# Optimization experiments

Measured on AMD Instinct MI355X. Metric: run time of the kernel, lower is better.

## Reference

```python
import jax, jax.numpy as jnp
import numpy as np

K = 5            # neighbors
TEMP = 1.0       # softmax temperature
BANK = 1000      # fixed bank capacity in source
B = 65536        # batch
D = 256          # feature_dim
EPS = 1e-12      # F.normalize eps


def _l2norm(x):
    # F.normalize(x, dim=1): x / max(||x||, eps)
    n = jnp.sqrt(jnp.sum(x * x, axis=1, keepdims=True))
    return x / jnp.maximum(n, EPS)


def setup_inputs() -> dict:
    key = jax.random.key(0)
    k1, k2, k3, k4 = jax.random.split(key, 4)
    features = jax.random.normal(k1, (B, D), dtype=jnp.float32)
    feature_bank = jax.random.normal(k2, (BANK, D), dtype=jnp.float32)
    # fusion_layer: Linear(2D -> D), ReLU, Linear(D -> D). torch weight layout [out, in].
    W1 = jax.random.normal(k3, (D, 2 * D), dtype=jnp.float32) * (1.0 / np.sqrt(2 * D))
    b1 = jnp.zeros((D,), dtype=jnp.float32)
    W2 = jax.random.normal(k4, (D, D), dtype=jnp.float32) * (1.0 / np.sqrt(D))
    b2 = jnp.zeros((D,), dtype=jnp.float32)
    return {"features": features, "feature_bank": feature_bank,
            "W1": W1, "b1": b1, "W2": W2, "b2": b2}


def reference(features, feature_bank, W1, b1, W2, b2):
    # knn_search: cosine similarity against the (full) bank
    qn = _l2norm(features)                      # [B, D]
    bn = _l2norm(feature_bank)                  # [BANK, D]
    sims = qn @ bn.T                            # [B, BANK]
    top_s, top_i = jax.lax.top_k(sims, K)       # [B, K]
    w = jax.nn.softmax(top_s / TEMP, axis=1)    # [B, K]
    neigh = feature_bank[top_i]                 # gather -> [B, K, D]
    nf = jnp.einsum('bkd,bk->bd', neigh, w)     # weighted average of neighbors
    # fusion MLP on concat([query, neighbors])
    fused = jnp.concatenate([features, nf], axis=1)    # [B, 2D]
    h = jax.nn.relu(fused @ W1.T + b1)                 # [B, D]
    out = h @ W2.T + b2                                # [B, D]
    return out
```

## Files before the change

### kernel.cpp

```cpp
#include <hip/hip_runtime.h>

#define DIM 256
#define NC 12

typedef __attribute__((ext_vector_type(8))) short short8;
typedef __attribute__((ext_vector_type(4))) float f32x4;

__device__ __forceinline__ short f32bf(float f) {
    unsigned u = __builtin_bit_cast(unsigned, f);
    unsigned r = u + 0x7FFFu + ((u >> 16) & 1u);
    return (short)(r >> 16);
}

__device__ __forceinline__ void gld_lds16(const void* g, void* l) {
    __builtin_amdgcn_global_load_lds((const __attribute__((address_space(1))) unsigned int*)g,
                                     (__attribute__((address_space(3))) unsigned int*)l, 16, 0, 0);
}

template<int CTRL>
__device__ __forceinline__ unsigned dppmax(unsigned x) {
    unsigned y = (unsigned)__builtin_amdgcn_update_dpp(0, (int)x, CTRL, 0xF, 0xF, true);
    return x > y ? x : y;
}

__global__ __launch_bounds__(256) void k_prep(const float* __restrict__ bank,
        const float* __restrict__ W1, const float* __restrict__ W2,
        short* __restrict__ bnbf, double* __restrict__ binv,
        short* __restrict__ w1bf, short* __restrict__ w2bf)
{
    __shared__ double part[4];
    __shared__ double s_inv;
    const int bid = blockIdx.x, t = threadIdx.x;
    if (bid < 1024) {
        const int row = bid;
        if (row < 1000) {
            float v = bank[(size_t)row * DIM + t];
            double ssq = (double)v * (double)v;
            for (int o = 32; o > 0; o >>= 1) ssq += __shfl_down(ssq, o);
            if ((t & 63) == 0) part[t >> 6] = ssq;
            __syncthreads();
            if (t == 0) {
                double s = part[0] + part[1] + part[2] + part[3];
                double n = sqrt(s); if (n < 1e-12) n = 1e-12;
                double inv = 1.0 / n;
                binv[row] = inv; s_inv = inv;
            }
            __syncthreads();
            const int pcol = (((t >> 3) ^ (row & 7)) << 3) | (t & 7);
            bnbf[(size_t)row * DIM + pcol] = f32bf((float)((double)v * s_inv));
        } else {
            bnbf[(size_t)row * DIM + t] = 0;
            if (t == 0) binv[row] = 0.0;
        }
    } else if (bid < 1536) {
        const int i = (bid - 1024) * 256 + t;
        w1bf[i] = f32bf(W1[i]);
    } else {
        const int i = (bid - 1536) * 256 + t;
        w2bf[i] = f32bf(W2[i]);
    }
}

__global__ __launch_bounds__(256) void k_sims(const float* __restrict__ feat,
        const short* __restrict__ bnbf, short* __restrict__ sims, int qoff)
{
    __shared__ alignas(16) short Qs[64 * 264];
    __shared__ alignas(16) short Ab[64 * 256];
    const int t = threadIdx.x, lane = t & 63, w = t >> 6;
    const int n16 = lane & 15, q4 = lane >> 4;

    {
        const int r = t >> 2, p = t & 3;
        const float4* src = (const float4*)(feat + (size_t)(qoff + blockIdx.x * 64 + r) * DIM + p * 64);
        short* dst = Qs + r * 264 + p * 64;
        #pragma unroll
        for (int i = 0; i < 16; ++i) {
            float4 v = src[i];
            dst[i*4+0] = f32bf(v.x); dst[i*4+1] = f32bf(v.y);
            dst[i*4+2] = f32bf(v.z); dst[i*4+3] = f32bf(v.w);
        }
    }
    const char* gA = (const char*)bnbf;
    char* lA = (char*)Ab;
    #pragma unroll
    for (int i = 0; i < 8; ++i)
        gld_lds16(gA + i * 4096 + t * 16, lA + i * 4096 + (t >> 6) * 1024);
    __syncthreads();

    short8 bq[8][4];
    #pragma unroll
    for (int kc = 0; kc < 8; ++kc)
        #pragma unroll
        for (int nt = 0; nt < 4; ++nt)
            bq[kc][nt] = *(const short8*)(Qs + (nt * 16 + n16) * 264 + kc * 32 + q4 * 8);

    const int ml = w * 16 + n16;
    int aoff[8];
    #pragma unroll
    for (int kc = 0; kc < 8; ++kc)
        aoff[kc] = (ml * 256 + (((kc * 4 + q4) ^ (ml & 7)) << 3)) * 2;

    const f32x4 vzero = {0.f, 0.f, 0.f, 0.f};
    for (int chunk = 0; chunk < 16; ++chunk) {
        f32x4 acc[4];
        acc[0] = vzero; acc[1] = vzero; acc[2] = vzero; acc[3] = vzero;
        #pragma unroll
        for (int kc = 0; kc < 8; ++kc) {
            short8 af = *(const short8*)(lA + aoff[kc]);
            #pragma unroll
            for (int nt = 0; nt < 4; ++nt)
                acc[nt] = __builtin_amdgcn_mfma_f32_16x16x32_bf16(af, bq[kc][nt], acc[nt], 0, 0, 0);
        }
        const int bankb = chunk * 64 + w * 16 + q4 * 4;
        #pragma unroll
        for (int nt = 0; nt < 4; ++nt) {
            const int qc = blockIdx.x * 64 + nt * 16 + n16;
            uint2 u;
            u.x = ((unsigned)(unsigned short)f32bf(acc[nt][0])) |
                  (((unsigned)(unsigned short)f32bf(acc[nt][1])) << 16);
            u.y = ((unsigned)(unsigned short)f32bf(acc[nt][2])) |
                  (((unsigned)(unsigned short)f32bf(acc[nt][3])) << 16);
            *(uint2*)(sims + (size_t)qc * 1024 + bankb) = u;
        }
        __syncthreads();
        if (chunk < 15) {
            #pragma unroll
            for (int i = 0; i < 8; ++i)
                gld_lds16(gA + (size_t)(chunk + 1) * 32768 + i * 4096 + t * 16,
                          lA + i * 4096 + (t >> 6) * 1024);
            __syncthreads();
        }
    }
}

__global__ __launch_bounds__(256) void k_select(const short* __restrict__ sims,
        int* __restrict__ top, int qoff)
{
    const int t = threadIdx.x, lane = t & 63, w = t >> 6;
    const int q = blockIdx.x * 4 + w;
    const uint4* p = (const uint4*)(sims + (size_t)q * 1024 + lane * 16);
    uint4 a = p[0], b = p[1];

    unsigned k[16];
    {
        unsigned words[8] = {a.x, a.y, a.z, a.w, b.x, b.y, b.z, b.w};
        #pragma unroll
        for (int j = 0; j < 16; ++j) {
            unsigned h = (j & 1) ? (words[j >> 1] >> 16) : (words[j >> 1] & 0xFFFFu);
            unsigned m = (h ^ 0x8000u) ^ ((0u - (h >> 15)) & 0x7FFFu);
            int idx = lane * 16 + j;
            k[j] = (idx < 1000) ? ((m << 16) | (unsigned)idx) : 0u;
        }
    }
    #pragma unroll
    for (int sz = 2; sz <= 16; sz <<= 1)
        #pragma unroll
        for (int st = sz >> 1; st >= 1; st >>= 1)
            #pragma unroll
            for (int i = 0; i < 16; ++i) {
                int j = i ^ st;
                if (j > i) {
                    bool desc = ((i & sz) == 0);
                    unsigned lo = k[i], hi = k[j];
                    unsigned mx = lo > hi ? lo : hi;
                    unsigned mn = lo > hi ? hi : lo;
                    k[i] = desc ? mx : mn;
                    k[j] = desc ? mn : mx;
                }
            }
    unsigned mine = 0;
    #pragma unroll
    for (int r = 0; r < 12; ++r) {
        unsigned m = k[0];
        m = dppmax<0xB1>(m);
        m = dppmax<0x4E>(m);
        m = dppmax<0x141>(m);
        m = dppmax<0x140>(m);
        m = dppmax<0x142>(m);
        m = dppmax<0x143>(m);
        unsigned wm = (unsigned)__builtin_amdgcn_readlane((int)m, 63);
        if (lane == r) mine = wm;
        if (k[0] == wm) {
            #pragma unroll
            for (int s = 0; s < 12; ++s) k[s] = k[s + 1];
        }
    }
    if (lane < 12) top[(size_t)(qoff + q) * NC + lane] = (int)(mine & 0xFFFFu);
}

__global__ __launch_bounds__(256) void k_refine(const float* __restrict__ feat,
        const float* __restrict__ bank, const int* __restrict__ top,
        const double* __restrict__ binv, short* __restrict__ nf)
{
    const int t = threadIdx.x, lane = t & 63, w = t >> 6;
    const int g = lane >> 4, u = lane & 15;
    const int q = blockIdx.x * 16 + w * 4 + g;

    int ci[NC];
    #pragma unroll
    for (int c = 0; c < NC; ++c) ci[c] = top[(size_t)q * NC + c];
    double bd[NC];
    #pragma unroll
    for (int c = 0; c < NC; ++c) bd[c] = binv[ci[c]];

    float qf[16];
    float ssf = 0.f;
    #pragma unroll
    for (int j = 0; j < 4; ++j) {
        float4 v = *(const float4*)(feat + (size_t)q * DIM + j * 64 + u * 4);
        qf[j*4+0] = v.x; qf[j*4+1] = v.y; qf[j*4+2] = v.z; qf[j*4+3] = v.w;
        ssf += v.x*v.x + v.y*v.y + v.z*v.z + v.w*v.w;
    }
    #pragma unroll
    for (int o = 1; o < 16; o <<= 1) ssf += __shfl_xor(ssf, o, 16);
    float nq = sqrtf(ssf); if (nq < 1e-12f) nq = 1e-12f;
    const float qi = 1.f / nq;

    float s[NC];
    #pragma unroll
    for (int c = 0; c < NC; ++c) {
        const float* brow = bank + (size_t)ci[c] * DIM + u * 4;
        float a0 = 0.f, a1 = 0.f, a2 = 0.f, a3 = 0.f;
        #pragma unroll
        for (int j = 0; j < 4; ++j) {
            float4 b = *(const float4*)(brow + j * 64);
            a0 += qf[j*4+0] * b.x; a1 += qf[j*4+1] * b.y;
            a2 += qf[j*4+2] * b.z; a3 += qf[j*4+3] * b.w;
        }
        s[c] = (a0 + a1) + (a2 + a3);
    }
    #pragma unroll
    for (int o = 1; o < 16; o <<= 1)
        #pragma unroll
        for (int c = 0; c < NC; ++c) s[c] += __shfl_xor(s[c], o, 16);

    float vf[NC];
    unsigned long long key[NC];
    #pragma unroll
    for (int c = 0; c < NC; ++c) {
        float v = s[c] * qi * (float)bd[c];
        vf[c] = v;
        unsigned ub = __builtin_bit_cast(unsigned, v);
        unsigned m = (ub >> 31) ? ~ub : (ub | 0x80000000u);
        key[c] = ((unsigned long long)m << 10) | (unsigned long long)(1023 - ci[c]);
    }

    int rank[NC];
    #pragma unroll
    for (int c = 0; c < NC; ++c) rank[c] = 0;
    #pragma unroll
    for (int c1 = 0; c1 < NC; ++c1)
        #pragma unroll
        for (int c2 = c1 + 1; c2 < NC; ++c2) {
            const bool gt = key[c1] > key[c2];
            rank[c2] += gt ? 1 : 0;
            rank[c1] += gt ? 0 : 1;
        }

    float v5 = 0.f, v6 = 0.f;
    #pragma unroll
    for (int c = 0; c < NC; ++c) {
        v5 += (rank[c] == 4) ? vf[c] : 0.f;
        v6 += (rank[c] == 5) ? vf[c] : 0.f;
    }
    const int need = (v5 - v6) < 1e-5f;
    if (__any(need)) {
        double ssd = 0.0;
        #pragma unroll
        for (int j = 0; j < 16; ++j) ssd += (double)qf[j] * (double)qf[j];
        #pragma unroll
        for (int o = 1; o < 16; o <<= 1) ssd += __shfl_xor(ssd, o, 16);
        double nd = sqrt(ssd); if (nd < 1e-12) nd = 1e-12;
        const double qid = 1.0 / nd;
        double sd[NC];
        #pragma unroll
        for (int c = 0; c < NC; ++c) {
            const float* brow = bank + (size_t)ci[c] * DIM + u * 4;
            double a0 = 0, a1 = 0, a2 = 0, a3 = 0;
            #pragma unroll
            for (int j = 0; j < 4; ++j) {
                float4 b = *(const float4*)(brow + j * 64);
                a0 += (double)qf[j*4+0] * b.x; a1 += (double)qf[j*4+1] * b.y;
                a2 += (double)qf[j*4+2] * b.z; a3 += (double)qf[j*4+3] * b.w;
            }
            sd[c] = (a0 + a1) + (a2 + a3);
        }
        #pragma unroll
        for (int o = 1; o < 16; o <<= 1)
            #pragma unroll
            for (int c = 0; c < NC; ++c) sd[c] += __shfl_xor(sd[c], o, 16);
        #pragma unroll
        for (int c = 0; c < NC; ++c) {
            double vd = sd[c] * qid * bd[c];
            vf[c] = (float)vd;
            unsigned long long ub = __builtin_bit_cast(unsigned long long, vd);
            unsigned long long m = (ub >> 63) ? ~ub : (ub | 0x8000000000000000ULL);
            key[c] = (m & ~0x3FFULL) | (unsigned long long)(1023 - ci[c]);
        }
        #pragma unroll
        for (int c = 0; c < NC; ++c) rank[c] = 0;
        #pragma unroll
        for (int c1 = 0; c1 < NC; ++c1)
            #pragma unroll
            for (int c2 = c1 + 1; c2 < NC; ++c2) {
                const bool gt = key[c1] > key[c2];
                rank[c2] += gt ? 1 : 0;
                rank[c1] += gt ? 0 : 1;
            }
    }

    float vm = vf[0];
    #pragma unroll
    for (int c = 1; c < NC; ++c) vm = fmaxf(vm, vf[c]);
    float e[NC]; float wsum = 0.f;
    #pragma unroll
    for (int c = 0; c < NC; ++c) {
        float ex = __expf(vf[c] - vm);
        ex = (rank[c] < 5) ? ex : 0.f;
        e[c] = ex; wsum += ex;
    }
    const float inv = 1.f / wsum;

    int   selidx[5];
    float selw[5];
    #pragma unroll
    for (int k = 0; k < 5; ++k) {
        int idx = 0; float wv = 0.f;
        #pragma unroll
        for (int c = 0; c < NC; ++c) {
            const bool is = (rank[c] == k);
            idx += is ? ci[c] : 0;
            wv  += is ? e[c]  : 0.f;
        }
        selidx[k] = idx; selw[k] = wv * inv;
    }

    float4 oa[4];
    #pragma unroll
    for (int j = 0; j < 4; ++j) { oa[j].x = 0.f; oa[j].y = 0.f; oa[j].z = 0.f; oa[j].w = 0.f; }
    #pragma unroll
    for (int k = 0; k < 5; ++k) {
        const float wc = selw[k];
        const float* brow = bank + (size_t)selidx[k] * DIM + u * 4;
        #pragma unroll
        for (int j = 0; j < 4; ++j) {
            float4 b = *(const float4*)(brow + j * 64);
            oa[j].x += wc * b.x; oa[j].y += wc * b.y;
            oa[j].z += wc * b.z; oa[j].w += wc * b.w;
        }
    }
    short* od = nf + (size_t)q * DIM + u * 4;
    #pragma unroll
    for (int j = 0; j < 4; ++j) {
        uint2 pk;
        pk.x = ((unsigned)(unsigned short)f32bf(oa[j].x)) |
               (((unsigned)(unsigned short)f32bf(oa[j].y)) << 16);
        pk.y = ((unsigned)(unsigned short)f32bf(oa[j].z)) |
               (((unsigned)(unsigned short)f32bf(oa[j].w)) << 16);
        *(uint2*)(od + j * 64) = pk;
    }
}

__global__ __launch_bounds__(256) void k_mlp1(const float* __restrict__ feat,
        const short* __restrict__ nf, const short* __restrict__ w1bf,
        const float* __restrict__ b1, short* __restrict__ h)
{
    __shared__ alignas(16) short As[64 * 40];
    __shared__ alignas(16) short Bs[256 * 40];
    const int t = threadIdx.x, lane = t & 63, w = t >> 6;
    const int mb = blockIdx.x * 64;
    const int r = t >> 2, p = t & 3;
    const int n16 = lane & 15, ko = (lane >> 4) << 3;
    const f32x4 vzero = {0.f, 0.f, 0.f, 0.f};

    f32x4 acc[4][4];
    #pragma unroll
    for (int a = 0; a < 4; ++a)
        #pragma unroll
        for (int b = 0; b < 4; ++b) acc[a][b] = vzero;

    for (int kc = 0; kc < 16; ++kc) {
        short* ad = As + r * 40 + p * 8;
        if (kc < 8) {
            const float4* s = (const float4*)(feat + (size_t)(mb + r) * 256 + kc * 32 + p * 8);
            float4 v0 = s[0], v1 = s[1];
            ad[0] = f32bf(v0.x); ad[1] = f32bf(v0.y); ad[2] = f32bf(v0.z); ad[3] = f32bf(v0.w);
            ad[4] = f32bf(v1.x); ad[5] = f32bf(v1.y); ad[6] = f32bf(v1.z); ad[7] = f32bf(v1.w);
        } else {
            *(uint4*)ad = *(const uint4*)(nf + (size_t)(mb + r) * 256 + (kc - 8) * 32 + p * 8);
        }
        {
            const uint4* bsrc = (const uint4*)(w1bf + (size_t)t * 512 + kc * 32);
            short* bdst = Bs + t * 40;
            *(uint4*)(bdst +  0) = bsrc[0];
            *(uint4*)(bdst +  8) = bsrc[1];
            *(uint4*)(bdst + 16) = bsrc[2];
            *(uint4*)(bdst + 24) = bsrc[3];
        }
        __syncthreads();
        short8 af[4], bf[4];
        #pragma unroll
        for (int mt = 0; mt < 4; ++mt)
            af[mt] = *(const short8*)(As + (mt * 16 + n16) * 40 + ko);
        #pragma unroll
        for (int nt = 0; nt < 4; ++nt)
            bf[nt] = *(const short8*)(Bs + (w * 64 + nt * 16 + n16) * 40 + ko);
        #pragma unroll
        for (int mt = 0; mt < 4; ++mt)
            #pragma unroll
            for (int nt = 0; nt < 4; ++nt)
                acc[mt][nt] = __builtin_amdgcn_mfma_f32_16x16x32_bf16(af[mt], bf[nt], acc[mt][nt], 0, 0, 0);
        __syncthreads();
    }
    {
        const int rq = (lane >> 4) << 2;
        const int cc = lane & 15;
        #pragma unroll
        for (int mt = 0; mt < 4; ++mt)
            #pragma unroll
            for (int nt = 0; nt < 4; ++nt) {
                const int row = mb + mt * 16 + rq;
                const int col = w * 64 + nt * 16 + cc;
                const float bias = b1[col];
                #pragma unroll
                for (int rr = 0; rr < 4; ++rr) {
                    float v = acc[mt][nt][rr] + bias;
                    v = fmaxf(v, 0.f);
                    h[(size_t)(row + rr) * 256 + col] = f32bf(v);
                }
            }
    }
}

__global__ __launch_bounds__(256) void k_mlp2(const short* __restrict__ h,
        const short* __restrict__ w2bf, const float* __restrict__ b2,
        float* __restrict__ out)
{
    __shared__ alignas(16) short As[64 * 40];
    __shared__ alignas(16) short Bs[256 * 40];
    const int t = threadIdx.x, lane = t & 63, w = t >> 6;
    const int mb = blockIdx.x * 64;
    const int r = t >> 2, p = t & 3;
    const int n16 = lane & 15, ko = (lane >> 4) << 3;
    const f32x4 vzero = {0.f, 0.f, 0.f, 0.f};

    f32x4 acc[4][4];
    #pragma unroll
    for (int a = 0; a < 4; ++a)
        #pragma unroll
        for (int b = 0; b < 4; ++b) acc[a][b] = vzero;

    for (int kc = 0; kc < 8; ++kc) {
        *(uint4*)(As + r * 40 + p * 8) =
            *(const uint4*)(h + (size_t)(mb + r) * 256 + kc * 32 + p * 8);
        {
            const uint4* bsrc = (const uint4*)(w2bf + (size_t)t * 256 + kc * 32);
            short* bdst = Bs + t * 40;
            *(uint4*)(bdst +  0) = bsrc[0];
            *(uint4*)(bdst +  8) = bsrc[1];
            *(uint4*)(bdst + 16) = bsrc[2];
            *(uint4*)(bdst + 24) = bsrc[3];
        }
        __syncthreads();
        short8 af[4], bf[4];
        #pragma unroll
        for (int mt = 0; mt < 4; ++mt)
            af[mt] = *(const short8*)(As + (mt * 16 + n16) * 40 + ko);
        #pragma unroll
        for (int nt = 0; nt < 4; ++nt)
            bf[nt] = *(const short8*)(Bs + (w * 64 + nt * 16 + n16) * 40 + ko);
        #pragma unroll
        for (int mt = 0; mt < 4; ++mt)
            #pragma unroll
            for (int nt = 0; nt < 4; ++nt)
                acc[mt][nt] = __builtin_amdgcn_mfma_f32_16x16x32_bf16(af[mt], bf[nt], acc[mt][nt], 0, 0, 0);
        __syncthreads();
    }
    {
        const int rq = (lane >> 4) << 2;
        const int cc = lane & 15;
        #pragma unroll
        for (int mt = 0; mt < 4; ++mt)
            #pragma unroll
            for (int nt = 0; nt < 4; ++nt) {
                const int row = mb + mt * 16 + rq;
                const int col = w * 64 + nt * 16 + cc;
                const float bias = b2[col];
                #pragma unroll
                for (int rr = 0; rr < 4; ++rr)
                    out[(size_t)(row + rr) * 256 + col] = acc[mt][nt][rr] + bias;
            }
    }
}

extern "C" void kernel_launch(void* const* d_in, const int* in_sizes, int n_in,
                              void* d_out, int out_size, void* d_ws, size_t ws_size,
                              hipStream_t stream) {
    const float* feat = (const float*)d_in[0];
    const float* bank = (const float*)d_in[1];
    const float* W1   = (const float*)d_in[2];
    const float* b1   = (const float*)d_in[3];
    const float* W2   = (const float*)d_in[4];
    const float* b2   = (const float*)d_in[5];
    float* out = (float*)d_out;

    char* ws = (char*)d_ws;
    short*  bnbf = (short*)(ws + 0);
    double* binv = (double*)(ws + 524288);
    short*  w1bf = (short*)(ws + 532480);
    short*  w2bf = (short*)(ws + 794624);
    int*    top  = (int*)(ws + 925696);
    short*  nf   = (short*)(ws + 4071424);
    short*  X    = (short*)(ws + 37625856);

    k_prep<<<1792, 256, 0, stream>>>(bank, W1, W2, bnbf, binv, w1bf, w2bf);
    for (int s = 0; s < 4; ++s) {
        const int qoff = s * 16384;
        k_sims  <<<256,  256, 0, stream>>>(feat, bnbf, X, qoff);
        k_select<<<4096, 256, 0, stream>>>(X, top, qoff);
    }
    k_refine<<<4096, 256, 0, stream>>>(feat, bank, top, binv, nf);
    k_mlp1  <<<1024, 256, 0, stream>>>(feat, nf, w1bf, b1, (short*)X);
    k_mlp2  <<<1024, 256, 0, stream>>>((short*)X, w2bf, b2, out);
}
```

Baseline: 433.9 us.

## Fuse MLP layers via LDS hidden tile and centralize refine ranking per block

The two MLP kernels become one: the ReLU hidden activations for a 64-row tile stay in shared memory (bf16) and feed the second GEMM directly, so the hidden tensor no longer makes a round trip through global memory and one launch is dropped. In k_refine, candidate indices and bank norms are staged in LDS once per block. The per-query ranking, softmax and selection now run on 16 threads instead of redundantly on all 16 lanes of each query group. The double-precision fallback threshold is tightened to 2e-6, which runs the fallback less often but adds syncs, serializes ranking on few threads and grows LDS use in the MLP kernel, which may lower occupancy.

Measured after the change: 407.5 us. -6.1%, faster.

```diff
diff --git a/kernel.cpp b/kernel.cpp
--- a/kernel.cpp
+++ b/kernel.cpp
@@ -192,16 +192,33 @@
         const float* __restrict__ bank, const int* __restrict__ top,
         const double* __restrict__ binv, short* __restrict__ nf)
 {
+    __shared__ int    cidxL[16 * NC];
+    __shared__ float  bdF[16 * NC];
+    __shared__ double bdD[16 * NC];
+    __shared__ float  simsF[16 * NC];
+    __shared__ double simsD[16 * NC];
+    __shared__ float  qiL[16];
+    __shared__ int    flagL[16];
+    __shared__ int    selidx[16][5];
+    __shared__ float  selw[16][5];
+
     const int t = threadIdx.x, lane = t & 63, w = t >> 6;
     const int g = lane >> 4, u = lane & 15;
-    const int q = blockIdx.x * 16 + w * 4 + g;
+    const int ql = w * 4 + g;
+    const int qbase = blockIdx.x * 16;
+    const int q = qbase + ql;
+
+    if (t < 16 * NC) {
+        const int c = top[(size_t)qbase * NC + t];
+        cidxL[t] = c;
+        const double b = binv[c];
+        bdD[t] = b; bdF[t] = (float)b;
+    }
+    __syncthreads();
 
     int ci[NC];
     #pragma unroll
-    for (int c = 0; c < NC; ++c) ci[c] = top[(size_t)q * NC + c];
-    double bd[NC];
-    #pragma unroll
-    for (int c = 0; c < NC; ++c) bd[c] = binv[ci[c]];
+    for (int c = 0; c < NC; ++c) ci[c] = cidxL[ql * NC + c];
 
     float qf[16];
     float ssf = 0.f;
@@ -214,7 +231,7 @@
     #pragma unroll
     for (int o = 1; o < 16; o <<= 1) ssf += __shfl_xor(ssf, o, 16);
     float nq = sqrtf(ssf); if (nq < 1e-12f) nq = 1e-12f;
-    const float qi = 1.f / nq;
+    if (u == 0) qiL[ql] = 1.f / nq;
 
     float s[NC];
     #pragma unroll
@@ -233,38 +250,69 @@
     for (int o = 1; o < 16; o <<= 1)
         #pragma unroll
         for (int c = 0; c < NC; ++c) s[c] += __shfl_xor(s[c], o, 16);
-
-    float vf[NC];
-    unsigned long long key[NC];
-    #pragma unroll
-    for (int c = 0; c < NC; ++c) {
-        float v = s[c] * qi * (float)bd[c];
-        vf[c] = v;
-        unsigned ub = __builtin_bit_cast(unsigned, v);
-        unsigned m = (ub >> 31) ? ~ub : (ub | 0x80000000u);
-        key[c] = ((unsigned long long)m << 10) | (unsigned long long)(1023 - ci[c]);
-    }
-
-    int rank[NC];
-    #pragma unroll
-    for (int c = 0; c < NC; ++c) rank[c] = 0;
-    #pragma unroll
-    for (int c1 = 0; c1 < NC; ++c1)
-        #pragma unroll
-        for (int c2 = c1 + 1; c2 < NC; ++c2) {
-            const bool gt = key[c1] > key[c2];
-            rank[c2] += gt ? 1 : 0;
-            rank[c1] += gt ? 0 : 1;
-        }
-
-    float v5 = 0.f, v6 = 0.f;
-    #pragma unroll
-    for (int c = 0; c < NC; ++c) {
-        v5 += (rank[c] == 4) ? vf[c] : 0.f;
-        v6 += (rank[c] == 5) ? vf[c] : 0.f;
-    }
-    const int need = (v5 - v6) < 1e-5f;
-    if (__any(need)) {
+    #pragma unroll
+    for (int c = 0; c < NC; ++c) if (u == c) simsF[ql * NC + c] = s[c];
+    __syncthreads();
+
+    if (t < 16) {
+        const float qi2 = qiL[t];
+        float vf[NC];
+        unsigned long long key[NC];
+        int cid[NC];
+        #pragma unroll
+        for (int c = 0; c < NC; ++c) {
+            cid[c] = cidxL[t * NC + c];
+            float v = simsF[t * NC + c] * qi2 * bdF[t * NC + c];
+            vf[c] = v;
+            unsigned ub = __builtin_bit_cast(unsigned, v);
+            unsigned m = (ub >> 31) ? ~ub : (ub | 0x80000000u);
+            key[c] = ((unsigned long long)m << 10) | (unsigned long long)(1023 - cid[c]);
+        }
+        int rank[NC];
+        #pragma unroll
+        for (int c = 0; c < NC; ++c) rank[c] = 0;
+        #pragma unroll
+        for (int c1 = 0; c1 < NC; ++c1)
+            #pragma unroll
+            for (int c2 = c1 + 1; c2 < NC; ++c2) {
+                const bool gt = key[c1] > key[c2];
+                rank[c2] += gt ? 1 : 0;
+                rank[c1] += gt ? 0 : 1;
+            }
+        float v5 = 0.f, v6 = 0.f;
+        #pragma unroll
+        for (int c = 0; c < NC; ++c) {
+            v5 += (rank[c] == 4) ? vf[c] : 0.f;
+            v6 += (rank[c] == 5) ? vf[c] : 0.f;
+        }
+        flagL[t] = (v5 - v6) < 2e-6f;
+
+        float vm = vf[0];
+        #pragma unroll
+        for (int c = 1; c < NC; ++c) vm = fmaxf(vm, vf[c]);
+        float e[NC]; float wsum = 0.f;
+        #pragma unroll
+        for (int c = 0; c < NC; ++c) {
+            float ex = __expf(vf[c] - vm);
+            ex = (rank[c] < 5) ? ex : 0.f;
+            e[c] = ex; wsum += ex;
+        }
+        const float inv = 1.f / wsum;
+        #pragma unroll
+        for (int k = 0; k < 5; ++k) {
+            int idx = 0; float wv = 0.f;
+            #pragma unroll
+            for (int c = 0; c < NC; ++c) {
+                const bool is = (rank[c] == k);
+                idx += is ? cid[c] : 0;
+                wv  += is ? e[c]  : 0.f;
+            }
+            selidx[t][k] = idx; selw[t][k] = wv * inv;
+        }
+    }
+    __syncthreads();
+
+    if (flagL[ql]) {
         double ssd = 0.0;
         #pragma unroll
         for (int j = 0; j < 16; ++j) ssd += (double)qf[j] * (double)qf[j];
@@ -290,13 +338,25 @@
             #pragma unroll
             for (int c = 0; c < NC; ++c) sd[c] += __shfl_xor(sd[c], o, 16);
         #pragma unroll
+        for (int c = 0; c < NC; ++c)
+            if (u == c) simsD[ql * NC + c] = sd[c] * qid * bdD[ql * NC + c];
+    }
+    __syncthreads();
+
+    if (t < 16 && flagL[t]) {
+        double vd[NC];
+        unsigned long long key[NC];
+        int cid[NC];
+        #pragma unroll
         for (int c = 0; c < NC; ++c) {
-            double vd = sd[c] * qid * bd[c];
-            vf[c] = (float)vd;
-            unsigned long long ub = __builtin_bit_cast(unsigned long long, vd);
+            cid[c] = cidxL[t * NC + c];
+            double v = simsD[t * NC + c];
+            vd[c] = v;
+            unsigned long long ub = __builtin_bit_cast(unsigned long long, v);
             unsigned long long m = (ub >> 63) ? ~ub : (ub | 0x8000000000000000ULL);
-            key[c] = (m & ~0x3FFULL) | (unsigned long long)(1023 - ci[c]);
-        }
+            key[c] = (m & ~0x3FFULL) | (unsigned long long)(1023 - cid[c]);
+        }
+        int rank[NC];
         #pragma unroll
         for (int c = 0; c < NC; ++c) rank[c] = 0;
         #pragma unroll
@@ -307,41 +367,44 @@
                 rank[c2] += gt ? 1 : 0;
                 rank[c1] += gt ? 0 : 1;
             }
-    }
-
-    float vm = vf[0];
-    #pragma unroll
-    for (int c = 1; c < NC; ++c) vm = fmaxf(vm, vf[c]);
-    float e[NC]; float wsum = 0.f;
-    #pragma unroll
-    for (int c = 0; c < NC; ++c) {
-        float ex = __expf(vf[c] - vm);
-        ex = (rank[c] < 5) ? ex : 0.f;
-        e[c] = ex; wsum += ex;
-    }
-    const float inv = 1.f / wsum;
-
-    int   selidx[5];
-    float selw[5];
+        float vf[NC];
+        #pragma unroll
+        for (int c = 0; c < NC; ++c) vf[c] = (float)vd[c];
+        float vm = vf[0];
+        #pragma unroll
+        for (int c = 1; c < NC; ++c) vm = fmaxf(vm, vf[c]);
+        float e[NC]; float wsum = 0.f;
+        #pragma unroll
+        for (int c = 0; c < NC; ++c) {
+            float ex = __expf(vf[c] - vm);
+            ex = (rank[c] < 5) ? ex : 0.f;
+            e[c] = ex; wsum += ex;
+        }
+        const float inv = 1.f / wsum;
+        #pragma unroll
+        for (int k = 0; k < 5; ++k) {
+            int idx = 0; float wv = 0.f;
+            #pragma unroll
+            for (int c = 0; c < NC; ++c) {
+                const bool is = (rank[c] == k);
+                idx += is ? cid[c] : 0;
+                wv  += is ? e[c]  : 0.f;
+            }
+            selidx[t][k] = idx; selw[t][k] = wv * inv;
+        }
+    }
+    __syncthreads();
+
+    float wk[5]; int ik[5];
+    #pragma unroll
+    for (int k = 0; k < 5; ++k) { wk[k] = selw[ql][k]; ik[k] = selidx[ql][k]; }
+    float4 oa[4];
+    #pragma unroll
+    for (int j = 0; j < 4; ++j) { oa[j].x = 0.f; oa[j].y = 0.f; oa[j].z = 0.f; oa[j].w = 0.f; }
     #pragma unroll
     for (int k = 0; k < 5; ++k) {
-        int idx = 0; float wv = 0.f;
-        #pragma unroll
-        for (int c = 0; c < NC; ++c) {
-            const bool is = (rank[c] == k);
-            idx += is ? ci[c] : 0;
-            wv  += is ? e[c]  : 0.f;
-        }
-        selidx[k] = idx; selw[k] = wv * inv;
-    }
-
-    float4 oa[4];
-    #pragma unroll
-    for (int j = 0; j < 4; ++j) { oa[j].x = 0.f; oa[j].y = 0.f; oa[j].z = 0.f; oa[j].w = 0.f; }
-    #pragma unroll
-    for (int k = 0; k < 5; ++k) {
-        const float wc = selw[k];
-        const float* brow = bank + (size_t)selidx[k] * DIM + u * 4;
+        const float wc = wk[k];
+        const float* brow = bank + (size_t)ik[k] * DIM + u * 4;
         #pragma unroll
         for (int j = 0; j < 4; ++j) {
             float4 b = *(const float4*)(brow + j * 64);
@@ -361,16 +424,19 @@
     }
 }
 
-__global__ __launch_bounds__(256) void k_mlp1(const float* __restrict__ feat,
+__global__ __launch_bounds__(256) void k_mlp(const float* __restrict__ feat,
         const short* __restrict__ nf, const short* __restrict__ w1bf,
-        const float* __restrict__ b1, short* __restrict__ h)
+        const short* __restrict__ w2bf, const float* __restrict__ b1,
+        const float* __restrict__ b2, float* __restrict__ out)
 {
     __shared__ alignas(16) short As[64 * 40];
     __shared__ alignas(16) short Bs[256 * 40];
+    __shared__ alignas(16) short Hs[64 * 264];
     const int t = threadIdx.x, lane = t & 63, w = t >> 6;
     const int mb = blockIdx.x * 64;
     const int r = t >> 2, p = t & 3;
     const int n16 = lane & 15, ko = (lane >> 4) << 3;
+    const int rq = (lane >> 4) << 2, cc = lane & 15;
     const f32x4 vzero = {0.f, 0.f, 0.f, 0.f};
 
     f32x4 acc[4][4];
@@ -412,47 +478,26 @@
                 acc[mt][nt] = __builtin_amdgcn_mfma_f32_16x16x32_bf16(af[mt], bf[nt], acc[mt][nt], 0, 0, 0);
         __syncthreads();
     }
-    {
-        const int rq = (lane >> 4) << 2;
-        const int cc = lane & 15;
-        #pragma unroll
-        for (int mt = 0; mt < 4; ++mt)
-            #pragma unroll
-            for (int nt = 0; nt < 4; ++nt) {
-                const int row = mb + mt * 16 + rq;
-                const int col = w * 64 + nt * 16 + cc;
-                const float bias = b1[col];
-                #pragma unroll
-                for (int rr = 0; rr < 4; ++rr) {
-                    float v = acc[mt][nt][rr] + bias;
-                    v = fmaxf(v, 0.f);
-                    h[(size_t)(row + rr) * 256 + col] = f32bf(v);
-                }
-            }
-    }
-}
-
-__global__ __launch_bounds__(256) void k_mlp2(const short* __restrict__ h,
-        const short* __restrict__ w2bf, const float* __restrict__ b2,
-        float* __restrict__ out)
-{
-    __shared__ alignas(16) short As[64 * 40];
-    __shared__ alignas(16) short Bs[256 * 40];
-    const int t = threadIdx.x, lane = t & 63, w = t >> 6;
-    const int mb = blockIdx.x * 64;
-    const int r = t >> 2, p = t & 3;
-    const int n16 = lane & 15, ko = (lane >> 4) << 3;
-    const f32x4 vzero = {0.f, 0.f, 0.f, 0.f};
-
-    f32x4 acc[4][4];
+    #pragma unroll
+    for (int mt = 0; mt < 4; ++mt)
+        #pragma unroll
+        for (int nt = 0; nt < 4; ++nt) {
+            const int row = mt * 16 + rq;
+            const int col = w * 64 + nt * 16 + cc;
+            const float bias = b1[col];
+            #pragma unroll
+            for (int rr = 0; rr < 4; ++rr) {
+                float v = acc[mt][nt][rr] + bias;
+                Hs[(row + rr) * 264 + col] = f32bf(fmaxf(v, 0.f));
+            }
+        }
     #pragma unroll
     for (int a = 0; a < 4; ++a)
         #pragma unroll
         for (int b = 0; b < 4; ++b) acc[a][b] = vzero;
+    __syncthreads();
 
     for (int kc = 0; kc < 8; ++kc) {
-        *(uint4*)(As + r * 40 + p * 8) =
-            *(const uint4*)(h + (size_t)(mb + r) * 256 + kc * 32 + p * 8);
         {
             const uint4* bsrc = (const uint4*)(w2bf + (size_t)t * 256 + kc * 32);
             short* bdst = Bs + t * 40;
@@ -465,7 +510,7 @@
         short8 af[4], bf[4];
         #pragma unroll
         for (int mt = 0; mt < 4; ++mt)
-            af[mt] = *(const short8*)(As + (mt * 16 + n16) * 40 + ko);
+            af[mt] = *(const short8*)(Hs + (mt * 16 + n16) * 264 + kc * 32 + ko);
         #pragma unroll
         for (int nt = 0; nt < 4; ++nt)
             bf[nt] = *(const short8*)(Bs + (w * 64 + nt * 16 + n16) * 40 + ko);
@@ -476,21 +521,17 @@
                 acc[mt][nt] = __builtin_amdgcn_mfma_f32_16x16x32_bf16(af[mt], bf[nt], acc[mt][nt], 0, 0, 0);
         __syncthreads();
     }
-    {
-        const int rq = (lane >> 4) << 2;
-        const int cc = lane & 15;
-        #pragma unroll
-        for (int mt = 0; mt < 4; ++mt)
-            #pragma unroll
-            for (int nt = 0; nt < 4; ++nt) {
-                const int row = mb + mt * 16 + rq;
-                const int col = w * 64 + nt * 16 + cc;
-                const float bias = b2[col];
-                #pragma unroll
-                for (int rr = 0; rr < 4; ++rr)
-                    out[(size_t)(row + rr) * 256 + col] = acc[mt][nt][rr] + bias;
-            }
-    }
+    #pragma unroll
+    for (int mt = 0; mt < 4; ++mt)
+        #pragma unroll
+        for (int nt = 0; nt < 4; ++nt) {
+            const int row = mb + mt * 16 + rq;
+            const int col = w * 64 + nt * 16 + cc;
+            const float bias = b2[col];
+            #pragma unroll
+            for (int rr = 0; rr < 4; ++rr)
+                out[(size_t)(row + rr) * 256 + col] = acc[mt][nt][rr] + bias;
+        }
 }
 
 extern "C" void kernel_launch(void* const* d_in, const int* in_sizes, int n_in,
@@ -520,6 +561,5 @@
         k_select<<<4096, 256, 0, stream>>>(X, top, qoff);
     }
     k_refine<<<4096, 256, 0, stream>>>(feat, bank, top, binv, nf);
-    k_mlp1  <<<1024, 256, 0, stream>>>(feat, nf, w1bf, b1, (short*)X);
-    k_mlp2  <<<1024, 256, 0, stream>>>((short*)X, w2bf, b2, out);
-}
+    k_mlp   <<<1024, 256, 0, stream>>>(feat, nf, w1bf, w2bf, b1, b2, out);
+}
```
